# Kernel tuning notes

Measured on AMD Instinct MI355X. Metric: run time of the kernel, lower is better.

## Reference

```python
import jax, jax.numpy as jnp
import numpy as np

N_HEADS = 8
N_GROUPS = 32
EPS = 1e-5


def setup_inputs() -> dict:
    key = jax.random.key(0)
    ks = jax.random.split(key, 3)
    b, c, h, w = 8, 512, 32, 32
    x = jax.random.normal(ks[0], (b, c, h, w), dtype=jnp.float32)
    gamma = jnp.ones((c,), jnp.float32)
    beta = jnp.zeros((c,), jnp.float32)
    w_qkv = jax.random.normal(ks[1], (3 * c, c), jnp.float32) * (1.0 / np.sqrt(c))
    b_qkv = jnp.zeros((3 * c,), jnp.float32)
    w_proj = jax.random.normal(ks[2], (c, c), jnp.float32) * (1.0 / np.sqrt(c))
    b_proj = jnp.zeros((c,), jnp.float32)
    return {"x": x, "gamma": gamma, "beta": beta, "w_qkv": w_qkv,
            "b_qkv": b_qkv, "w_proj": w_proj, "b_proj": b_proj}


def _group_norm(x, gamma, beta):
    # x: [b, c, T]; GroupNorm over (c//G, T) per group, computed in fp32
    b, c, t = x.shape
    xg = x.reshape(b, N_GROUPS, c // N_GROUPS, t).astype(jnp.float32)
    mean = xg.mean(axis=(2, 3), keepdims=True)
    var = xg.var(axis=(2, 3), keepdims=True)
    xg = (xg - mean) * jax.lax.rsqrt(var + EPS)
    xn = xg.reshape(b, c, t).astype(x.dtype)
    return xn * gamma[None, :, None] + beta[None, :, None]


def reference(x, gamma, beta, w_qkv, b_qkv, w_proj, b_proj):
    b, c, *spatial = x.shape
    t = int(np.prod(spatial))
    xf = x.reshape(b, c, t)
    h = _group_norm(xf, gamma, beta)
    # 1x1 conv == channel matmul
    qkv = jnp.einsum('oc,bct->bot', w_qkv, h) + b_qkv[None, :, None]  # [b, 3c, t]
    ch = c // N_HEADS
    qkv = qkv.reshape(b * N_HEADS, 3 * ch, t)
    q, k, v = qkv[:, :ch], qkv[:, ch:2 * ch], qkv[:, 2 * ch:]
    scale = 1.0 / np.sqrt(np.sqrt(ch))
    weight = jnp.einsum('bct,bcs->bts', q * scale, k * scale)
    weight = jax.nn.softmax(weight.astype(jnp.float32), axis=-1).astype(weight.dtype)
    a = jnp.einsum('bts,bcs->bct', weight, v)  # [b*H, ch, t]
    a = a.reshape(b, c, t)
    h = jnp.einsum('oc,bct->bot', w_proj, a) + b_proj[None, :, None]
    return (xf + h).reshape(b, c, *spatial)
```

## Files before the change

kernel.cpp:

```cpp
#include <hip/hip_runtime.h>
#include <hip/hip_bf16.h>
#include <math.h>

#define BATCH 8
#define CDIM 512
#define TDIM 1024
#define NHD 8

typedef __attribute__((ext_vector_type(8))) short bf16x8;
typedef __attribute__((ext_vector_type(8))) _Float16 f16x8;
typedef __attribute__((ext_vector_type(4))) float floatx4;

#define QSCALE 0.18033688011112042f

static __device__ __forceinline__ unsigned short f2bf(float f) {
    __hip_bfloat16 h = __float2bfloat16(f);
    return *reinterpret_cast<unsigned short*>(&h);
}
static __device__ __forceinline__ unsigned short f2h(float f) {
    _Float16 h = (_Float16)f;
    return *reinterpret_cast<unsigned short*>(&h);
}
static __device__ __forceinline__ void async_load16(const unsigned short* gsrc,
                                                    unsigned short* ldst) {
    __builtin_amdgcn_global_load_lds(
        (const __attribute__((address_space(1))) void*)gsrc,
        (__attribute__((address_space(3))) void*)ldst, 16, 0, 0);
}

__global__ __launch_bounds__(256) void cvt2_kernel(const float* __restrict__ a,
                                                   const float* __restrict__ b,
                                                   unsigned short* __restrict__ da,
                                                   unsigned short* __restrict__ db) {
    int i = blockIdx.x * 256 + threadIdx.x;
    const int nA = 1536 * 512 / 4;
    const float* s;
    unsigned short* d;
    int j;
    if (i < nA) { s = a; d = da; j = i; }
    else        { s = b; d = db; j = i - nA; }
    float4 v = ((const float4*)s)[j];
    ushort4 o;
    o.x = f2bf(v.x); o.y = f2bf(v.y); o.z = f2bf(v.z); o.w = f2bf(v.w);
    ((ushort4*)d)[j] = o;
}

__global__ __launch_bounds__(256) void gn_kernel(const float* __restrict__ x,
                                                 const float* __restrict__ gamma,
                                                 const float* __restrict__ beta,
                                                 unsigned short* __restrict__ h_t) {
    int bg = blockIdx.x;
    int b = bg >> 5, g = bg & 31;
    const float* xp = x + ((size_t)(b * CDIM + g * 16)) * TDIM;
    int tid = threadIdx.x;

    float s = 0.f, ss = 0.f;
    for (int r = 0; r < 16; ++r) {
        float4 v = ((const float4*)xp)[r * 256 + tid];
        s  += v.x + v.y + v.z + v.w;
        ss += v.x * v.x + v.y * v.y + v.z * v.z + v.w * v.w;
    }
    for (int off = 32; off > 0; off >>= 1) {
        s  += __shfl_down(s, off, 64);
        ss += __shfl_down(ss, off, 64);
    }
    __shared__ float rs[4], rss[4], stat[2];
    int wave = tid >> 6;
    if ((tid & 63) == 0) { rs[wave] = s; rss[wave] = ss; }
    __syncthreads();
    if (tid == 0) {
        float S  = rs[0] + rs[1] + rs[2] + rs[3];
        float SS = rss[0] + rss[1] + rss[2] + rss[3];
        float mean = S * (1.f / 16384.f);
        float var  = SS * (1.f / 16384.f) - mean * mean;
        stat[0] = mean;
        stat[1] = rsqrtf(var + 1e-5f);
    }
    __syncthreads();
    float mean = stat[0], rstd = stat[1];

    int cpair = tid & 7, trow = tid >> 3;
    int c0 = g * 16 + cpair * 2;
    float g0 = gamma[c0] * rstd,  g1 = gamma[c0 + 1] * rstd;
    float b0 = beta[c0] - mean * g0, b1 = beta[c0 + 1] - mean * g1;
    const float* x0 = x + ((size_t)(b * CDIM + c0)) * TDIM;
    const float* x1 = x0 + TDIM;
    unsigned int* hp = (unsigned int*)h_t + (size_t)b * TDIM * 256 + g * 8 + cpair;
    for (int p = 0; p < 32; ++p) {
        int t = p * 32 + trow;
        float v0 = x0[t] * g0 + b0;
        float v1 = x1[t] * g1 + b1;
        hp[(size_t)t * 256] = (unsigned)f2bf(v0) | ((unsigned)f2bf(v1) << 16);
    }
}

__global__ __launch_bounds__(256) void mfma_gemm(
    const unsigned short* __restrict__ Wb,
    const unsigned short* __restrict__ Xt,
    const float* __restrict__ bias,
    int M, int K, int mode,
    unsigned short* __restrict__ q_t,
    unsigned short* __restrict__ k_t,
    unsigned short* __restrict__ v,
    const float* __restrict__ resid,
    float* __restrict__ outp) {
    __shared__ __align__(16) unsigned short As[128 * 32];
    __shared__ __align__(16) unsigned short Bs[128 * 32];

    int tid = threadIdx.x;
    int n0 = blockIdx.x * 128, m0 = blockIdx.y * 128, bb = blockIdx.z;
    const unsigned short* Xp = Xt + (size_t)bb * TDIM * K;

    int lane = tid & 63, w = tid >> 6;
    int l15 = lane & 15, quad = lane >> 4;
    int wm = w >> 1, wn = w & 1;

    int s0i = w * 128 + lane;
    int rA0 = s0i >> 2, gA0 = s0i & 3;
    int rA1 = (s0i + 64) >> 2, gA1 = (s0i + 64) & 3;
    const unsigned short* aS0 = Wb + (size_t)(m0 + rA0) * K + gA0 * 8;
    const unsigned short* aS1 = Wb + (size_t)(m0 + rA1) * K + gA1 * 8;
    const unsigned short* bS0 = Xp + (size_t)(n0 + rA0) * K + gA0 * 8;
    const unsigned short* bS1 = Xp + (size_t)(n0 + rA1) * K + gA1 * 8;
    unsigned short* aD0 = &As[(w * 128) * 8];
    unsigned short* aD1 = &As[(w * 128 + 64) * 8];
    unsigned short* bD0 = &Bs[(w * 128) * 8];
    unsigned short* bD1 = &Bs[(w * 128 + 64) * 8];

    floatx4 acc[4][4];
#pragma unroll
    for (int i = 0; i < 4; ++i)
#pragma unroll
        for (int j = 0; j < 4; ++j) acc[i][j] = (floatx4){0.f, 0.f, 0.f, 0.f};

    for (int k0 = 0; k0 < K; k0 += 32) {
        async_load16(aS0 + k0, aD0);
        async_load16(aS1 + k0, aD1);
        async_load16(bS0 + k0, bD0);
        async_load16(bS1 + k0, bD1);
        __syncthreads();

        bf16x8 af[4], bfr[4];
#pragma unroll
        for (int mi = 0; mi < 4; ++mi)
            af[mi] = *(const bf16x8*)&As[(wm * 64 + mi * 16 + l15) * 32 + quad * 8];
#pragma unroll
        for (int ni = 0; ni < 4; ++ni)
            bfr[ni] = *(const bf16x8*)&Bs[(wn * 64 + ni * 16 + l15) * 32 + quad * 8];
#pragma unroll
        for (int mi = 0; mi < 4; ++mi)
#pragma unroll
            for (int ni = 0; ni < 4; ++ni)
                acc[mi][ni] = __builtin_amdgcn_mfma_f32_16x16x32_bf16(
                    af[mi], bfr[ni], acc[mi][ni], 0, 0, 0);
        __syncthreads();
    }

    int b8 = bb * NHD;
#pragma unroll
    for (int mi = 0; mi < 4; ++mi) {
        int mBase = m0 + wm * 64 + mi * 16 + quad * 4;
#pragma unroll
        for (int ni = 0; ni < 4; ++ni) {
            floatx4 a = acc[mi][ni];
            int n = n0 + wn * 64 + ni * 16 + l15;
            if (mode == 0) {
                int chunk = mBase >> 6;
                int hd = chunk / 3, part = chunk % 3;
                int cB = mBase & 63;
#pragma unroll
                for (int r = 0; r < 4; ++r) {
                    float val = a[r] + bias[mBase + r];
                    int c = cB + r;
                    if (part == 0)
                        q_t[((size_t)(b8 + hd) * TDIM + n) * 64 + c] = f2h(val * QSCALE);
                    else if (part == 1)
                        k_t[((size_t)(b8 + hd) * TDIM + n) * 64 + c] = f2h(val);
                    else
                        v[((size_t)(b8 + hd) * 64 + c) * TDIM + n] = f2h(val);
                }
            } else {
                size_t base = ((size_t)bb * CDIM + mBase) * TDIM + n;
#pragma unroll
                for (int r = 0; r < 4; ++r)
                    outp[base + (size_t)r * TDIM] =
                        a[r] + bias[mBase + r] + resid[base + (size_t)r * TDIM];
            }
        }
    }
}

__global__ __launch_bounds__(256, 4) void attn_kernel(
    const unsigned short* __restrict__ q_t,
    const unsigned short* __restrict__ k_t,
    const unsigned short* __restrict__ v,
    unsigned short* __restrict__ a_t) {
    __shared__ __align__(16) unsigned short Qs[64 * 64];
    __shared__ __align__(16) unsigned short Ks[64 * 64];
    __shared__ __align__(16) unsigned short Vs[64 * 64];

    int tid = threadIdx.x;
    int q0 = blockIdx.x * 64;
    int bh = blockIdx.y;
    int lane = tid & 63, w = tid >> 6;
    int l15 = lane & 15, quad = lane >> 4;
    int l7 = l15 & 7;

    const unsigned short* Qp = q_t + (size_t)bh * TDIM * 64;
    const unsigned short* Kp = k_t + (size_t)bh * TDIM * 64;
    const unsigned short* Vp = v + (size_t)bh * 64 * TDIM;

#pragma unroll
    for (int it = 0; it < 2; ++it) {
        int s = it * 256 + tid;
        int r = s >> 3, gs = s & 7, g = gs ^ (r & 7);
        *(uint4*)&Qs[s * 8] = *(const uint4*)(Qp + (size_t)(q0 + r) * 64 + g * 8);
    }

    int kofs[2], vofs[2];
    unsigned short *kdst[2], *vdst[2];
#pragma unroll
    for (int c = 0; c < 2; ++c) {
        int s = w * 128 + c * 64 + lane;
        int m = s >> 3, gs = s & 7, g = gs ^ (m & 7);
        int mi = m >> 4, qq = (m >> 2) & 3, rr = m & 3;
        int pm = (mi & 1) * 32 + qq * 8 + (mi >> 1) * 4 + rr;
        kofs[c] = pm * 64 + g * 8;
        vofs[c] = m * TDIM + g * 8;
        kdst[c] = &Ks[(w * 128 + c * 64) * 8];
        vdst[c] = &Vs[(w * 128 + c * 64) * 8];
    }

    __syncthreads();
    int myrow = w * 16 + l15;
    f16x8 qf[2];
#pragma unroll
    for (int ch = 0; ch < 2; ++ch)
        qf[ch] = *(const f16x8*)&Qs[myrow * 64 + ((ch * 4 + quad) ^ l7) * 8];

    floatx4 o_acc[4];
#pragma unroll
    for (int i = 0; i < 4; ++i) o_acc[i] = (floatx4){0.f, 0.f, 0.f, 0.f};
    float m_run = -INFINITY, l_run = 0.f;

    for (int s0 = 0; s0 < TDIM; s0 += 64) {
        async_load16(Kp + (size_t)s0 * 64 + kofs[0], kdst[0]);
        async_load16(Kp + (size_t)s0 * 64 + kofs[1], kdst[1]);
        async_load16(Vp + s0 + vofs[0], vdst[0]);
        async_load16(Vp + s0 + vofs[1], vdst[1]);
        __syncthreads();

        floatx4 sT[4];
#pragma unroll
        for (int mi = 0; mi < 4; ++mi) {
            int row = mi * 16 + l15;
            f16x8 k0 = *(const f16x8*)&Ks[row * 64 + ((0 + quad) ^ l7) * 8];
            f16x8 k1 = *(const f16x8*)&Ks[row * 64 + ((4 + quad) ^ l7) * 8];
            floatx4 z = (floatx4){0.f, 0.f, 0.f, 0.f};
            z = __builtin_amdgcn_mfma_f32_16x16x32_f16(k0, qf[0], z, 0, 0, 0);
            z = __builtin_amdgcn_mfma_f32_16x16x32_f16(k1, qf[1], z, 0, 0, 0);
            sT[mi] = z;
        }

        float mx = sT[0][0];
#pragma unroll
        for (int mi = 0; mi < 4; ++mi)
#pragma unroll
            for (int r = 0; r < 4; ++r) mx = fmaxf(mx, sT[mi][r]);
        mx = fmaxf(mx, __shfl_xor(mx, 16));
        mx = fmaxf(mx, __shfl_xor(mx, 32));
        float mn = fmaxf(m_run, mx);
        float alpha = __builtin_amdgcn_exp2f(m_run - mn);
        float sum = 0.f;
#pragma unroll
        for (int mi = 0; mi < 4; ++mi)
#pragma unroll
            for (int r = 0; r < 4; ++r) {
                float p = __builtin_amdgcn_exp2f(sT[mi][r] - mn);
                sT[mi][r] = p;
                sum += p;
            }
        sum += __shfl_xor(sum, 16);
        sum += __shfl_xor(sum, 32);
        l_run = l_run * alpha + sum;
        m_run = mn;

        f16x8 pf[2];
#pragma unroll
        for (int kb = 0; kb < 2; ++kb) {
            pf[kb][0] = (_Float16)sT[kb][0];
            pf[kb][1] = (_Float16)sT[kb][1];
            pf[kb][2] = (_Float16)sT[kb][2];
            pf[kb][3] = (_Float16)sT[kb][3];
            pf[kb][4] = (_Float16)sT[kb + 2][0];
            pf[kb][5] = (_Float16)sT[kb + 2][1];
            pf[kb][6] = (_Float16)sT[kb + 2][2];
            pf[kb][7] = (_Float16)sT[kb + 2][3];
        }

#pragma unroll
        for (int ci = 0; ci < 4; ++ci) {
            o_acc[ci][0] *= alpha; o_acc[ci][1] *= alpha;
            o_acc[ci][2] *= alpha; o_acc[ci][3] *= alpha;
        }
#pragma unroll
        for (int ci = 0; ci < 4; ++ci) {
            int row = ci * 16 + l15;
#pragma unroll
            for (int kb = 0; kb < 2; ++kb) {
                f16x8 vf = *(const f16x8*)&Vs[row * 64 + ((kb * 4 + quad) ^ l7) * 8];
                o_acc[ci] = __builtin_amdgcn_mfma_f32_16x16x32_f16(vf, pf[kb], o_acc[ci], 0, 0, 0);
            }
        }
        __syncthreads();
    }

    float linv = 1.f / l_run;
#pragma unroll
    for (int ci = 0; ci < 4; ++ci) {
        ushort4 pk;
        pk.x = f2bf(o_acc[ci][0] * linv);
        pk.y = f2bf(o_acc[ci][1] * linv);
        pk.z = f2bf(o_acc[ci][2] * linv);
        pk.w = f2bf(o_acc[ci][3] * linv);
        int col = ci * 16 + quad * 4;
        int gs = (col >> 3) ^ l7;
        *(ushort4*)&Ks[myrow * 64 + gs * 8 + (quad & 1) * 4] = pk;
    }
    __syncthreads();
    int b = bh >> 3, hd = bh & 7;
    size_t obase = ((size_t)b * TDIM + q0) * CDIM + hd * 64;
#pragma unroll
    for (int it = 0; it < 2; ++it) {
        int s = it * 256 + tid;
        int r = s >> 3, gs = s & 7, g = gs ^ (r & 7);
        *(uint4*)(a_t + obase + (size_t)r * CDIM + g * 8) = *(const uint4*)&Ks[s * 8];
    }
}

extern "C" void kernel_launch(void* const* d_in, const int* in_sizes, int n_in,
                              void* d_out, int out_size, void* d_ws, size_t ws_size,
                              hipStream_t stream) {
    (void)in_sizes; (void)n_in; (void)out_size; (void)ws_size;
    const float* x      = (const float*)d_in[0];
    const float* gamma  = (const float*)d_in[1];
    const float* beta   = (const float*)d_in[2];
    const float* w_qkv  = (const float*)d_in[3];
    const float* b_qkv  = (const float*)d_in[4];
    const float* w_proj = (const float*)d_in[5];
    const float* b_proj = (const float*)d_in[6];
    float* out = (float*)d_out;

    unsigned short* wqkv_bf  = (unsigned short*)d_ws;
    unsigned short* wproj_bf = wqkv_bf + 1536 * 512;
    unsigned short* h_t      = wproj_bf + 512 * 512;
    unsigned short* q_t      = h_t + (size_t)BATCH * TDIM * CDIM;
    unsigned short* k_t      = q_t + (size_t)64 * TDIM * 64;
    unsigned short* vv       = k_t + (size_t)64 * TDIM * 64;
    unsigned short* a_t      = vv + (size_t)64 * TDIM * 64;

    cvt2_kernel<<<(1536 * 512 + 512 * 512) / 1024, 256, 0, stream>>>(
        w_qkv, w_proj, wqkv_bf, wproj_bf);

    gn_kernel<<<BATCH * 32, 256, 0, stream>>>(x, gamma, beta, h_t);

    mfma_gemm<<<dim3(8, 12, BATCH), 256, 0, stream>>>(
        wqkv_bf, h_t, b_qkv, 1536, 512, 0, q_t, k_t, vv, nullptr, nullptr);

    attn_kernel<<<dim3(16, 64), 256, 0, stream>>>(q_t, k_t, vv, a_t);

    mfma_gemm<<<dim3(8, 4, BATCH), 256, 0, stream>>>(
        wproj_bf, a_t, b_proj, 512, 512, 1, nullptr, nullptr, nullptr, x, out);
}
```

Before: 178.8 us.

## Merge prep kernels, switch to fp16, deepen GEMM K-step, retile attention per block

Merges the weight conversion and group-norm kernels into one launch and switches all intermediates from bf16 to fp16. The GEMM now loads 64 wide K slices per barrier. The attention kernel handles 256 queries per block with double-buffered async K/V loads, so each K/V tile is reused across four query fragments, and it writes output directly instead of staging it through LDS. The trade-offs are far fewer attention blocks (256), higher register pressure at occupancy 1, and fp16 range risk on intermediates.

```diff
diff --git a/kernel.cpp b/kernel.cpp
--- a/kernel.cpp
+++ b/kernel.cpp
@@ -7,16 +7,11 @@
 #define TDIM 1024
 #define NHD 8
 
-typedef __attribute__((ext_vector_type(8))) short bf16x8;
 typedef __attribute__((ext_vector_type(8))) _Float16 f16x8;
 typedef __attribute__((ext_vector_type(4))) float floatx4;
 
 #define QSCALE 0.18033688011112042f
 
-static __device__ __forceinline__ unsigned short f2bf(float f) {
-    __hip_bfloat16 h = __float2bfloat16(f);
-    return *reinterpret_cast<unsigned short*>(&h);
-}
 static __device__ __forceinline__ unsigned short f2h(float f) {
     _Float16 h = (_Float16)f;
     return *reinterpret_cast<unsigned short*>(&h);
@@ -28,31 +23,29 @@
         (__attribute__((address_space(3))) void*)ldst, 16, 0, 0);
 }
 
-__global__ __launch_bounds__(256) void cvt2_kernel(const float* __restrict__ a,
-                                                   const float* __restrict__ b,
-                                                   unsigned short* __restrict__ da,
-                                                   unsigned short* __restrict__ db) {
-    int i = blockIdx.x * 256 + threadIdx.x;
-    const int nA = 1536 * 512 / 4;
-    const float* s;
-    unsigned short* d;
-    int j;
-    if (i < nA) { s = a; d = da; j = i; }
-    else        { s = b; d = db; j = i - nA; }
-    float4 v = ((const float4*)s)[j];
-    ushort4 o;
-    o.x = f2bf(v.x); o.y = f2bf(v.y); o.z = f2bf(v.z); o.w = f2bf(v.w);
-    ((ushort4*)d)[j] = o;
-}
-
-__global__ __launch_bounds__(256) void gn_kernel(const float* __restrict__ x,
-                                                 const float* __restrict__ gamma,
-                                                 const float* __restrict__ beta,
-                                                 unsigned short* __restrict__ h_t) {
+__global__ __launch_bounds__(256) void prep_kernel(
+    const float* __restrict__ x, const float* __restrict__ gamma,
+    const float* __restrict__ beta, const float* __restrict__ w_qkv,
+    const float* __restrict__ w_proj, unsigned short* __restrict__ h_t,
+    unsigned short* __restrict__ wq, unsigned short* __restrict__ wp) {
+    int tid = threadIdx.x;
+    if (blockIdx.x >= 256) {
+        int i = (blockIdx.x - 256) * 256 + tid;
+        const int nA = 1536 * 512 / 4;
+        const float* s;
+        unsigned short* d;
+        int j;
+        if (i < nA) { s = w_qkv; d = wq; j = i; }
+        else        { s = w_proj; d = wp; j = i - nA; }
+        float4 v = ((const float4*)s)[j];
+        ushort4 o;
+        o.x = f2h(v.x); o.y = f2h(v.y); o.z = f2h(v.z); o.w = f2h(v.w);
+        ((ushort4*)d)[j] = o;
+        return;
+    }
     int bg = blockIdx.x;
     int b = bg >> 5, g = bg & 31;
     const float* xp = x + ((size_t)(b * CDIM + g * 16)) * TDIM;
-    int tid = threadIdx.x;
 
     float s = 0.f, ss = 0.f;
     for (int r = 0; r < 16; ++r) {
@@ -90,7 +83,7 @@
         int t = p * 32 + trow;
         float v0 = x0[t] * g0 + b0;
         float v1 = x1[t] * g1 + b1;
-        hp[(size_t)t * 256] = (unsigned)f2bf(v0) | ((unsigned)f2bf(v1) << 16);
+        hp[(size_t)t * 256] = (unsigned)f2h(v0) | ((unsigned)f2h(v1) << 16);
     }
 }
 
@@ -104,8 +97,8 @@
     unsigned short* __restrict__ v,
     const float* __restrict__ resid,
     float* __restrict__ outp) {
-    __shared__ __align__(16) unsigned short As[128 * 32];
-    __shared__ __align__(16) unsigned short Bs[128 * 32];
+    __shared__ __align__(16) unsigned short As[2 * 128 * 32];
+    __shared__ __align__(16) unsigned short Bs[2 * 128 * 32];
 
     int tid = threadIdx.x;
     int n0 = blockIdx.x * 128, m0 = blockIdx.y * 128, bb = blockIdx.z;
@@ -115,17 +108,19 @@
     int l15 = lane & 15, quad = lane >> 4;
     int wm = w >> 1, wn = w & 1;
 
-    int s0i = w * 128 + lane;
-    int rA0 = s0i >> 2, gA0 = s0i & 3;
-    int rA1 = (s0i + 64) >> 2, gA1 = (s0i + 64) & 3;
-    const unsigned short* aS0 = Wb + (size_t)(m0 + rA0) * K + gA0 * 8;
-    const unsigned short* aS1 = Wb + (size_t)(m0 + rA1) * K + gA1 * 8;
-    const unsigned short* bS0 = Xp + (size_t)(n0 + rA0) * K + gA0 * 8;
-    const unsigned short* bS1 = Xp + (size_t)(n0 + rA1) * K + gA1 * 8;
-    unsigned short* aD0 = &As[(w * 128) * 8];
-    unsigned short* aD1 = &As[(w * 128 + 64) * 8];
-    unsigned short* bD0 = &Bs[(w * 128) * 8];
-    unsigned short* bD1 = &Bs[(w * 128 + 64) * 8];
+    const unsigned short* aSrc[4];
+    const unsigned short* bSrc[4];
+    unsigned short* aDst[4];
+    unsigned short* bDst[4];
+#pragma unroll
+    for (int c = 0; c < 4; ++c) {
+        int slot = w * 256 + c * 64 + lane;
+        int panel = slot >> 9, row = (slot >> 2) & 127, g4 = slot & 3;
+        aSrc[c] = Wb + (size_t)(m0 + row) * K + panel * 32 + g4 * 8;
+        bSrc[c] = Xp + (size_t)(n0 + row) * K + panel * 32 + g4 * 8;
+        aDst[c] = &As[(w * 256 + c * 64) * 8];
+        bDst[c] = &Bs[(w * 256 + c * 64) * 8];
+    }
 
     floatx4 acc[4][4];
 #pragma unroll
@@ -133,26 +128,29 @@
 #pragma unroll
         for (int j = 0; j < 4; ++j) acc[i][j] = (floatx4){0.f, 0.f, 0.f, 0.f};
 
-    for (int k0 = 0; k0 < K; k0 += 32) {
-        async_load16(aS0 + k0, aD0);
-        async_load16(aS1 + k0, aD1);
-        async_load16(bS0 + k0, bD0);
-        async_load16(bS1 + k0, bD1);
+    for (int k0 = 0; k0 < K; k0 += 64) {
+#pragma unroll
+        for (int c = 0; c < 4; ++c) {
+            async_load16(aSrc[c] + k0, aDst[c]);
+            async_load16(bSrc[c] + k0, bDst[c]);
+        }
         __syncthreads();
-
-        bf16x8 af[4], bfr[4];
-#pragma unroll
-        for (int mi = 0; mi < 4; ++mi)
-            af[mi] = *(const bf16x8*)&As[(wm * 64 + mi * 16 + l15) * 32 + quad * 8];
-#pragma unroll
-        for (int ni = 0; ni < 4; ++ni)
-            bfr[ni] = *(const bf16x8*)&Bs[(wn * 64 + ni * 16 + l15) * 32 + quad * 8];
-#pragma unroll
-        for (int mi = 0; mi < 4; ++mi)
+#pragma unroll
+        for (int kc = 0; kc < 2; ++kc) {
+            f16x8 af[4], bfr[4];
+#pragma unroll
+            for (int mi = 0; mi < 4; ++mi)
+                af[mi] = *(const f16x8*)&As[(kc * 128 + wm * 64 + mi * 16 + l15) * 32 + quad * 8];
 #pragma unroll
             for (int ni = 0; ni < 4; ++ni)
-                acc[mi][ni] = __builtin_amdgcn_mfma_f32_16x16x32_bf16(
-                    af[mi], bfr[ni], acc[mi][ni], 0, 0, 0);
+                bfr[ni] = *(const f16x8*)&Bs[(kc * 128 + wn * 64 + ni * 16 + l15) * 32 + quad * 8];
+#pragma unroll
+            for (int mi = 0; mi < 4; ++mi)
+#pragma unroll
+                for (int ni = 0; ni < 4; ++ni)
+                    acc[mi][ni] = __builtin_amdgcn_mfma_f32_16x16x32_f16(
+                        af[mi], bfr[ni], acc[mi][ni], 0, 0, 0);
+        }
         __syncthreads();
     }
 
@@ -168,16 +166,25 @@
                 int chunk = mBase >> 6;
                 int hd = chunk / 3, part = chunk % 3;
                 int cB = mBase & 63;
-#pragma unroll
-                for (int r = 0; r < 4; ++r) {
-                    float val = a[r] + bias[mBase + r];
-                    int c = cB + r;
-                    if (part == 0)
-                        q_t[((size_t)(b8 + hd) * TDIM + n) * 64 + c] = f2h(val * QSCALE);
-                    else if (part == 1)
-                        k_t[((size_t)(b8 + hd) * TDIM + n) * 64 + c] = f2h(val);
-                    else
-                        v[((size_t)(b8 + hd) * 64 + c) * TDIM + n] = f2h(val);
+                if (part == 0) {
+                    ushort4 pk;
+                    pk.x = f2h((a[0] + bias[mBase + 0]) * QSCALE);
+                    pk.y = f2h((a[1] + bias[mBase + 1]) * QSCALE);
+                    pk.z = f2h((a[2] + bias[mBase + 2]) * QSCALE);
+                    pk.w = f2h((a[3] + bias[mBase + 3]) * QSCALE);
+                    *(ushort4*)&q_t[((size_t)(b8 + hd) * TDIM + n) * 64 + cB] = pk;
+                } else if (part == 1) {
+                    ushort4 pk;
+                    pk.x = f2h(a[0] + bias[mBase + 0]);
+                    pk.y = f2h(a[1] + bias[mBase + 1]);
+                    pk.z = f2h(a[2] + bias[mBase + 2]);
+                    pk.w = f2h(a[3] + bias[mBase + 3]);
+                    *(ushort4*)&k_t[((size_t)(b8 + hd) * TDIM + n) * 64 + cB] = pk;
+                } else {
+#pragma unroll
+                    for (int r = 0; r < 4; ++r)
+                        v[((size_t)(b8 + hd) * 64 + cB + r) * TDIM + n] =
+                            f2h(a[r] + bias[mBase + r]);
                 }
             } else {
                 size_t base = ((size_t)bb * CDIM + mBase) * TDIM + n;
@@ -190,17 +197,17 @@
     }
 }
 
-__global__ __launch_bounds__(256, 4) void attn_kernel(
+__global__ __launch_bounds__(256, 1) void attn_kernel(
     const unsigned short* __restrict__ q_t,
     const unsigned short* __restrict__ k_t,
     const unsigned short* __restrict__ v,
     unsigned short* __restrict__ a_t) {
-    __shared__ __align__(16) unsigned short Qs[64 * 64];
-    __shared__ __align__(16) unsigned short Ks[64 * 64];
-    __shared__ __align__(16) unsigned short Vs[64 * 64];
+    __shared__ __align__(16) unsigned short Qs[256 * 64];
+    __shared__ __align__(16) unsigned short Kb[2][64 * 64];
+    __shared__ __align__(16) unsigned short Vb[2][64 * 64];
 
     int tid = threadIdx.x;
-    int q0 = blockIdx.x * 64;
+    int q0 = blockIdx.x * 256;
     int bh = blockIdx.y;
     int lane = tid & 63, w = tid >> 6;
     int l15 = lane & 15, quad = lane >> 4;
@@ -211,130 +218,147 @@
     const unsigned short* Vp = v + (size_t)bh * 64 * TDIM;
 
 #pragma unroll
-    for (int it = 0; it < 2; ++it) {
-        int s = it * 256 + tid;
-        int r = s >> 3, gs = s & 7, g = gs ^ (r & 7);
-        *(uint4*)&Qs[s * 8] = *(const uint4*)(Qp + (size_t)(q0 + r) * 64 + g * 8);
+    for (int c = 0; c < 8; ++c) {
+        int s_ = w * 512 + c * 64 + lane;
+        int r = s_ >> 3, gs = s_ & 7, g = gs ^ (r & 7);
+        async_load16(Qp + (size_t)(q0 + r) * 64 + g * 8, &Qs[(w * 512 + c * 64) * 8]);
     }
 
     int kofs[2], vofs[2];
-    unsigned short *kdst[2], *vdst[2];
+    unsigned short* kdst[2];
+    unsigned short* vdst[2];
 #pragma unroll
     for (int c = 0; c < 2; ++c) {
-        int s = w * 128 + c * 64 + lane;
-        int m = s >> 3, gs = s & 7, g = gs ^ (m & 7);
+        int s_ = w * 128 + c * 64 + lane;
+        int m = s_ >> 3, gs = s_ & 7, g = gs ^ (m & 7);
         int mi = m >> 4, qq = (m >> 2) & 3, rr = m & 3;
         int pm = (mi & 1) * 32 + qq * 8 + (mi >> 1) * 4 + rr;
         kofs[c] = pm * 64 + g * 8;
         vofs[c] = m * TDIM + g * 8;
-        kdst[c] = &Ks[(w * 128 + c * 64) * 8];
-        vdst[c] = &Vs[(w * 128 + c * 64) * 8];
-    }
-
+        kdst[c] = &Kb[0][(w * 128 + c * 64) * 8];
+        vdst[c] = &Vb[0][(w * 128 + c * 64) * 8];
+    }
+    const int bufstep = 64 * 64;
+
+#pragma unroll
+    for (int c = 0; c < 2; ++c) {
+        async_load16(Kp + kofs[c], kdst[c]);
+        async_load16(Vp + vofs[c], vdst[c]);
+    }
     __syncthreads();
-    int myrow = w * 16 + l15;
-    f16x8 qf[2];
-#pragma unroll
-    for (int ch = 0; ch < 2; ++ch)
-        qf[ch] = *(const f16x8*)&Qs[myrow * 64 + ((ch * 4 + quad) ^ l7) * 8];
-
-    floatx4 o_acc[4];
-#pragma unroll
-    for (int i = 0; i < 4; ++i) o_acc[i] = (floatx4){0.f, 0.f, 0.f, 0.f};
-    float m_run = -INFINITY, l_run = 0.f;
-
-    for (int s0 = 0; s0 < TDIM; s0 += 64) {
-        async_load16(Kp + (size_t)s0 * 64 + kofs[0], kdst[0]);
-        async_load16(Kp + (size_t)s0 * 64 + kofs[1], kdst[1]);
-        async_load16(Vp + s0 + vofs[0], vdst[0]);
-        async_load16(Vp + s0 + vofs[1], vdst[1]);
+
+    f16x8 qf[4][2];
+#pragma unroll
+    for (int f = 0; f < 4; ++f)
+#pragma unroll
+        for (int ch = 0; ch < 2; ++ch)
+            qf[f][ch] = *(const f16x8*)&Qs[(w * 64 + f * 16 + l15) * 64 +
+                                           ((ch * 4 + quad) ^ l7) * 8];
+
+    floatx4 o_acc[4][4];
+#pragma unroll
+    for (int i = 0; i < 4; ++i)
+#pragma unroll
+        for (int j = 0; j < 4; ++j) o_acc[i][j] = (floatx4){0.f, 0.f, 0.f, 0.f};
+    float m_run[4] = {-INFINITY, -INFINITY, -INFINITY, -INFINITY};
+    float l_run[4] = {0.f, 0.f, 0.f, 0.f};
+
+    for (int it = 0; it < 16; ++it) {
+        int cur = it & 1;
+        if (it < 15) {
+            int s0n = (it + 1) * 64;
+#pragma unroll
+            for (int c = 0; c < 2; ++c) {
+                async_load16(Kp + (size_t)s0n * 64 + kofs[c], kdst[c] + (cur ^ 1) * bufstep);
+                async_load16(Vp + s0n + vofs[c], vdst[c] + (cur ^ 1) * bufstep);
+            }
+        }
+        f16x8 kf[4][2], vf[4][2];
+#pragma unroll
+        for (int mi = 0; mi < 4; ++mi)
+#pragma unroll
+            for (int ch = 0; ch < 2; ++ch) {
+                int off = (mi * 16 + l15) * 64 + ((ch * 4 + quad) ^ l7) * 8;
+                kf[mi][ch] = *(const f16x8*)&Kb[cur][off];
+                vf[mi][ch] = *(const f16x8*)&Vb[cur][off];
+            }
+
+        f16x8 pf[4][2];
+#pragma unroll
+        for (int f = 0; f < 4; ++f) {
+            floatx4 sT[4];
+#pragma unroll
+            for (int mi = 0; mi < 4; ++mi) {
+                floatx4 z = (floatx4){0.f, 0.f, 0.f, 0.f};
+                z = __builtin_amdgcn_mfma_f32_16x16x32_f16(kf[mi][0], qf[f][0], z, 0, 0, 0);
+                z = __builtin_amdgcn_mfma_f32_16x16x32_f16(kf[mi][1], qf[f][1], z, 0, 0, 0);
+                sT[mi] = z;
+            }
+            float mx = sT[0][0];
+#pragma unroll
+            for (int mi = 0; mi < 4; ++mi)
+#pragma unroll
+                for (int r = 0; r < 4; ++r) mx = fmaxf(mx, sT[mi][r]);
+            mx = fmaxf(mx, __shfl_xor(mx, 16));
+            mx = fmaxf(mx, __shfl_xor(mx, 32));
+            float mn = fmaxf(m_run[f], mx);
+            float alpha = __builtin_amdgcn_exp2f(m_run[f] - mn);
+            float sum = 0.f;
+#pragma unroll
+            for (int mi = 0; mi < 4; ++mi)
+#pragma unroll
+                for (int r = 0; r < 4; ++r) {
+                    float p = __builtin_amdgcn_exp2f(sT[mi][r] - mn);
+                    sT[mi][r] = p;
+                    sum += p;
+                }
+            sum += __shfl_xor(sum, 16);
+            sum += __shfl_xor(sum, 32);
+            l_run[f] = l_run[f] * alpha + sum;
+            m_run[f] = mn;
+#pragma unroll
+            for (int ci = 0; ci < 4; ++ci) {
+                o_acc[ci][f][0] *= alpha; o_acc[ci][f][1] *= alpha;
+                o_acc[ci][f][2] *= alpha; o_acc[ci][f][3] *= alpha;
+            }
+#pragma unroll
+            for (int kb = 0; kb < 2; ++kb) {
+                pf[f][kb][0] = (_Float16)sT[kb][0];
+                pf[f][kb][1] = (_Float16)sT[kb][1];
+                pf[f][kb][2] = (_Float16)sT[kb][2];
+                pf[f][kb][3] = (_Float16)sT[kb][3];
+                pf[f][kb][4] = (_Float16)sT[kb + 2][0];
+                pf[f][kb][5] = (_Float16)sT[kb + 2][1];
+                pf[f][kb][6] = (_Float16)sT[kb + 2][2];
+                pf[f][kb][7] = (_Float16)sT[kb + 2][3];
+            }
+        }
+#pragma unroll
+        for (int ci = 0; ci < 4; ++ci)
+#pragma unroll
+            for (int f = 0; f < 4; ++f)
+#pragma unroll
+                for (int kb = 0; kb < 2; ++kb)
+                    o_acc[ci][f] = __builtin_amdgcn_mfma_f32_16x16x32_f16(
+                        vf[ci][kb], pf[f][kb], o_acc[ci][f], 0, 0, 0);
         __syncthreads();
-
-        floatx4 sT[4];
-#pragma unroll
-        for (int mi = 0; mi < 4; ++mi) {
-            int row = mi * 16 + l15;
-            f16x8 k0 = *(const f16x8*)&Ks[row * 64 + ((0 + quad) ^ l7) * 8];
-            f16x8 k1 = *(const f16x8*)&Ks[row * 64 + ((4 + quad) ^ l7) * 8];
-            floatx4 z = (floatx4){0.f, 0.f, 0.f, 0.f};
-            z = __builtin_amdgcn_mfma_f32_16x16x32_f16(k0, qf[0], z, 0, 0, 0);
-            z = __builtin_amdgcn_mfma_f32_16x16x32_f16(k1, qf[1], z, 0, 0, 0);
-            sT[mi] = z;
-        }
-
-        float mx = sT[0][0];
-#pragma unroll
-        for (int mi = 0; mi < 4; ++mi)
-#pragma unroll
-            for (int r = 0; r < 4; ++r) mx = fmaxf(mx, sT[mi][r]);
-        mx = fmaxf(mx, __shfl_xor(mx, 16));
-        mx = fmaxf(mx, __shfl_xor(mx, 32));
-        float mn = fmaxf(m_run, mx);
-        float alpha = __builtin_amdgcn_exp2f(m_run - mn);
-        float sum = 0.f;
-#pragma unroll
-        for (int mi = 0; mi < 4; ++mi)
-#pragma unroll
-            for (int r = 0; r < 4; ++r) {
-                float p = __builtin_amdgcn_exp2f(sT[mi][r] - mn);
-                sT[mi][r] = p;
-                sum += p;
-            }
-        sum += __shfl_xor(sum, 16);
-        sum += __shfl_xor(sum, 32);
-        l_run = l_run * alpha + sum;
-        m_run = mn;
-
-        f16x8 pf[2];
-#pragma unroll
-        for (int kb = 0; kb < 2; ++kb) {
-            pf[kb][0] = (_Float16)sT[kb][0];
-            pf[kb][1] = (_Float16)sT[kb][1];
-            pf[kb][2] = (_Float16)sT[kb][2];
-            pf[kb][3] = (_Float16)sT[kb][3];
-            pf[kb][4] = (_Float16)sT[kb + 2][0];
-            pf[kb][5] = (_Float16)sT[kb + 2][1];
-            pf[kb][6] = (_Float16)sT[kb + 2][2];
-            pf[kb][7] = (_Float16)sT[kb + 2][3];
-        }
-
+    }
+
+    int b = bh >> 3, hd = bh & 7;
+#pragma unroll
+    for (int f = 0; f < 4; ++f) {
+        float linv = 1.f / l_run[f];
+        int t = q0 + w * 64 + f * 16 + l15;
+        size_t rowb = ((size_t)b * TDIM + t) * CDIM + hd * 64 + quad * 4;
 #pragma unroll
         for (int ci = 0; ci < 4; ++ci) {
-            o_acc[ci][0] *= alpha; o_acc[ci][1] *= alpha;
-            o_acc[ci][2] *= alpha; o_acc[ci][3] *= alpha;
-        }
-#pragma unroll
-        for (int ci = 0; ci < 4; ++ci) {
-            int row = ci * 16 + l15;
-#pragma unroll
-            for (int kb = 0; kb < 2; ++kb) {
-                f16x8 vf = *(const f16x8*)&Vs[row * 64 + ((kb * 4 + quad) ^ l7) * 8];
-                o_acc[ci] = __builtin_amdgcn_mfma_f32_16x16x32_f16(vf, pf[kb], o_acc[ci], 0, 0, 0);
-            }
-        }
-        __syncthreads();
-    }
-
-    float linv = 1.f / l_run;
-#pragma unroll
-    for (int ci = 0; ci < 4; ++ci) {
-        ushort4 pk;
-        pk.x = f2bf(o_acc[ci][0] * linv);
-        pk.y = f2bf(o_acc[ci][1] * linv);
-        pk.z = f2bf(o_acc[ci][2] * linv);
-        pk.w = f2bf(o_acc[ci][3] * linv);
-        int col = ci * 16 + quad * 4;
-        int gs = (col >> 3) ^ l7;
-        *(ushort4*)&Ks[myrow * 64 + gs * 8 + (quad & 1) * 4] = pk;
-    }
-    __syncthreads();
-    int b = bh >> 3, hd = bh & 7;
-    size_t obase = ((size_t)b * TDIM + q0) * CDIM + hd * 64;
-#pragma unroll
-    for (int it = 0; it < 2; ++it) {
-        int s = it * 256 + tid;
-        int r = s >> 3, gs = s & 7, g = gs ^ (r & 7);
-        *(uint4*)(a_t + obase + (size_t)r * CDIM + g * 8) = *(const uint4*)&Ks[s * 8];
+            ushort4 pk;
+            pk.x = f2h(o_acc[ci][f][0] * linv);
+            pk.y = f2h(o_acc[ci][f][1] * linv);
+            pk.z = f2h(o_acc[ci][f][2] * linv);
+            pk.w = f2h(o_acc[ci][f][3] * linv);
+            *(ushort4*)&a_t[rowb + ci * 16] = pk;
+        }
     }
 }
 
@@ -351,24 +375,21 @@
     const float* b_proj = (const float*)d_in[6];
     float* out = (float*)d_out;
 
-    unsigned short* wqkv_bf  = (unsigned short*)d_ws;
-    unsigned short* wproj_bf = wqkv_bf + 1536 * 512;
-    unsigned short* h_t      = wproj_bf + 512 * 512;
-    unsigned short* q_t      = h_t + (size_t)BATCH * TDIM * CDIM;
-    unsigned short* k_t      = q_t + (size_t)64 * TDIM * 64;
-    unsigned short* vv       = k_t + (size_t)64 * TDIM * 64;
-    unsigned short* a_t      = vv + (size_t)64 * TDIM * 64;
-
-    cvt2_kernel<<<(1536 * 512 + 512 * 512) / 1024, 256, 0, stream>>>(
-        w_qkv, w_proj, wqkv_bf, wproj_bf);
-
-    gn_kernel<<<BATCH * 32, 256, 0, stream>>>(x, gamma, beta, h_t);
+    unsigned short* wq  = (unsigned short*)d_ws;
+    unsigned short* wp  = wq + 1536 * 512;
+    unsigned short* h_t = wp + 512 * 512;
+    unsigned short* q_t = h_t + (size_t)BATCH * TDIM * CDIM;
+    unsigned short* k_t = q_t + (size_t)64 * TDIM * 64;
+    unsigned short* vv  = k_t + (size_t)64 * TDIM * 64;
+    unsigned short* a_t = vv + (size_t)64 * TDIM * 64;
+
+    prep_kernel<<<1280, 256, 0, stream>>>(x, gamma, beta, w_qkv, w_proj, h_t, wq, wp);
 
     mfma_gemm<<<dim3(8, 12, BATCH), 256, 0, stream>>>(
-        wqkv_bf, h_t, b_qkv, 1536, 512, 0, q_t, k_t, vv, nullptr, nullptr);
-
-    attn_kernel<<<dim3(16, 64), 256, 0, stream>>>(q_t, k_t, vv, a_t);
+        wq, h_t, b_qkv, 1536, 512, 0, q_t, k_t, vv, nullptr, nullptr);
+
+    attn_kernel<<<dim3(4, 64), 256, 0, stream>>>(q_t, k_t, vv, a_t);
 
     mfma_gemm<<<dim3(8, 4, BATCH), 256, 0, stream>>>(
-        wproj_bf, a_t, b_proj, 512, 512, 1, nullptr, nullptr, nullptr, x, out);
-}
+        wp, a_t, b_proj, 512, 512, 1, nullptr, nullptr, nullptr, x, out);
+}
```

New measurement: 178.9 us. About the same (+0.1%).
